# Performance work log

Hardware: AMD Instinct MI355X
Metric: run time of the kernel (lower is better)

Reference implementation:

```python
import jax, jax.numpy as jnp
import numpy as np

N_SITES = 64
N_HALF = N_SITES // 2
D_BOND = 128
N_OUTPUT = 10
DIM = 2
BATCH = 128


def _initializer(key, n_sites, d_phys, d_bond):
    # identity cores + small noise, matching the numpy initializer
    w = jnp.broadcast_to(jnp.eye(d_bond, dtype=jnp.float32),
                         (d_phys, n_sites, d_bond, d_bond))
    return w + 0.01 * jax.random.normal(key, w.shape, dtype=jnp.float32)


def setup_inputs() -> dict:
    key = jax.random.key(0)
    k_in, k_l, k_r, k_m = jax.random.split(key, 4)
    inputs = jax.random.normal(k_in, (BATCH, N_SITES, DIM), dtype=jnp.float32)
    left = _initializer(k_l, N_HALF, DIM, D_BOND)            # [dim, n_half, D, D]
    right = _initializer(k_r, N_HALF, DIM, D_BOND)           # [dim, n_half, D, D]
    middle = _initializer(k_m, 1, N_OUTPUT, D_BOND)[:, 0]    # [n_output, D, D]
    return {"inputs": inputs, "left": left, "right": right, "middle": middle}


def _reduction(t):
    # t: [size, B, D, D] -> [B, D, D] via balanced binary-tree matmul chain
    size = t.shape[0]
    while size > 1:
        half = size // 2
        nice = 2 * half
        leftover = t[nice:]
        t = jnp.matmul(t[0:nice:2], t[1:nice:2])  # [half, B, D, D]
        if leftover.shape[0]:
            t = jnp.concatenate([t, leftover], axis=0)
        size = half + (size % 2)
    return t[0]


def reference(inputs, left, right, middle):
    n_half = left.shape[1]
    # contract physical legs: [dim, l, D, D] x [B, l, dim] -> [l, B, D, D]
    l = jnp.einsum('slij,bls->lbij', left, inputs[:, :n_half])
    r = jnp.einsum('slij,bls->lbij', right, inputs[:, n_half:])
    l = _reduction(l)  # [B, D, D]
    r = _reduction(r)  # [B, D, D]
    # close the ring through the output core
    return jnp.einsum('bij,cjk,bki->bc', l, middle, r)  # [B, n_output]
```

## Files before the change

### kernel.cpp

```cpp
#include <hip/hip_runtime.h>


typedef __attribute__((ext_vector_type(8))) short short8v;
typedef __attribute__((ext_vector_type(16))) float f32x16;

__device__ __forceinline__ unsigned cvt_pk_bf16(float lo, float hi) {
  unsigned r;
  asm("v_cvt_pk_bf16_f32 %0, %1, %2" : "=v"(r) : "v"(lo), "v"(hi));
  return r;
}

#define GLOAD_LDS16(g, l)                                          \
  __builtin_amdgcn_global_load_lds(                                \
      (const __attribute__((address_space(1))) void*)(g),          \
      (__attribute__((address_space(3))) void*)(l), 16, 0, 0)

__global__ __launch_bounds__(256) void make_dt(const float* __restrict__ left,
                                               const float* __restrict__ right,
                                               ushort* __restrict__ Dt) {
  __shared__ float lw[64 * 132];
  const int tid = threadIdx.x;
  const int mat = blockIdx.x >> 1;
  const int rh  = blockIdx.x & 1;
  const float* W = (mat >= 64 ? right : left) + (size_t)(mat & 63) * 16384 +
                   (size_t)rh * 8192;

#pragma unroll
  for (int it = 0; it < 8; ++it) {
    int g = it * 256 + tid;
    float4 v = *(const float4*)(W + g * 4);
    *(float4*)&lw[(g >> 5) * 132 + (g & 31) * 4] = v;
  }
  __syncthreads();

#pragma unroll
  for (int ff = 0; ff < 4; ++ff) {
    int f = ff * 256 + tid;
    int l = f & 63, mt = (f >> 6) & 3, ksl = f >> 8;
    int m = 32 * mt + (l & 31);
    int kbl = 16 * ksl + 8 * (l >> 5);
    float v[8];
#pragma unroll
    for (int j = 0; j < 8; ++j)
      v[j] = lw[(kbl + j) * 132 + m] - ((64 * rh + kbl + j == m) ? 1.0f : 0.0f);
    uint4 o;
    o.x = cvt_pk_bf16(v[0], v[1]);
    o.y = cvt_pk_bf16(v[2], v[3]);
    o.z = cvt_pk_bf16(v[4], v[5]);
    o.w = cvt_pk_bf16(v[6], v[7]);
    *(uint4*)(Dt + (size_t)mat * 16384 +
              (size_t)(((4 * rh + ksl) * 4 + mt) * 64 + l) * 8) = o;
  }
}

__global__ __launch_bounds__(256, 1) void mps_chain_mfma(
    const float* __restrict__ inp, const float* __restrict__ left,
    const float* __restrict__ right, const ushort* __restrict__ Dt,
    float* __restrict__ res) {
  __shared__ ushort ldsD[2][32768];
  __shared__ float xs[64];

  const int tid  = threadIdx.x;
  const int half = blockIdx.x >> 7;
  const int b    = blockIdx.x & 127;
  const int lane = tid & 63;
  const int w    = tid >> 6;
  const int c    = lane & 31;
  const int hi   = lane >> 5;
  const int cg   = 32 * w + c;
  const int wofs = w * 512;

  if (tid < 64) xs[tid] = inp[b * 128 + half * 64 + tid];

  const ushort* DtH = Dt + (size_t)(half * 2) * 32 * 16384;

  __syncthreads();

#pragma unroll
  for (int p = 0; p < 2; ++p) {
    const ushort* gp = DtH + (size_t)(p * 32 + 1) * 16384;
#pragma unroll
    for (int i = 0; i < 8; ++i)
      GLOAD_LDS16(gp + i * 2048 + wofs + lane * 8,
                  &ldsD[0][p * 16384 + i * 2048 + wofs]);
  }

  f32x16 acc[4];

  {
    const float* Wg = half ? right : left;
    const float x0 = xs[0], x1 = xs[1];
#pragma unroll
    for (int t = 0; t < 4; ++t)
#pragma unroll
      for (int g = 0; g < 4; ++g) {
        const int row = 32 * t + 8 * g + 4 * hi;
        const float4 w0 = *(const float4*)(Wg + cg * 128 + row);
        const float4 w1 = *(const float4*)(Wg + 32 * 16384 + cg * 128 + row);
        acc[t][4 * g + 0] = x0 * w0.x + x1 * w1.x;
        acc[t][4 * g + 1] = x0 * w0.y + x1 * w1.y;
        acc[t][4 * g + 2] = x0 * w0.z + x1 * w1.z;
        acc[t][4 * g + 3] = x0 * w0.w + x1 * w1.w;
      }
  }

  __syncthreads();

  int cur = 0;
  for (int s = 1; s < 32; ++s) {
    const float x0 = xs[2 * s], x1 = xs[2 * s + 1];
    const float s01 = x0 + x1;

    if (s < 31) {
#pragma unroll
      for (int p = 0; p < 2; ++p) {
        const ushort* gp = DtH + (size_t)(p * 32 + s + 1) * 16384;
#pragma unroll
        for (int i = 0; i < 8; ++i)
          GLOAD_LDS16(gp + i * 2048 + wofs + lane * 8,
                      &ldsD[cur ^ 1][p * 16384 + i * 2048 + wofs]);
      }
    }

    f32x16 tn[4];
#pragma unroll
    for (int t = 0; t < 4; ++t)
#pragma unroll
      for (int r = 0; r < 16; ++r) tn[t][r] = s01 * acc[t][r];

#pragma unroll
    for (int ks = 0; ks < 8; ++ks) {
      const int t = ks >> 1, q = ks & 1;
#pragma unroll
      for (int r = 0; r < 4; ++r) {
        float a  = acc[t][q * 8 + r];
        float b2 = acc[t][q * 8 + 4 + r];
        asm volatile("v_permlane32_swap_b32 %0, %1" : "+v"(a), "+v"(b2));
        acc[t][q * 8 + r]     = a;
        acc[t][q * 8 + 4 + r] = b2;
      }
      uint4 p0, p1;
      {
        const float* v = (const float*)&acc[t] + q * 8;
        p0.x = cvt_pk_bf16(x0 * v[0], x0 * v[1]);
        p0.y = cvt_pk_bf16(x0 * v[2], x0 * v[3]);
        p0.z = cvt_pk_bf16(x0 * v[4], x0 * v[5]);
        p0.w = cvt_pk_bf16(x0 * v[6], x0 * v[7]);
        p1.x = cvt_pk_bf16(x1 * v[0], x1 * v[1]);
        p1.y = cvt_pk_bf16(x1 * v[2], x1 * v[3]);
        p1.z = cvt_pk_bf16(x1 * v[4], x1 * v[5]);
        p1.w = cvt_pk_bf16(x1 * v[6], x1 * v[7]);
      }
      const short8v y0 = __builtin_bit_cast(short8v, p0);
      const short8v y1 = __builtin_bit_cast(short8v, p1);
#pragma unroll
      for (int mt = 0; mt < 4; ++mt) {
        short8v d0 = *(const short8v*)&ldsD[cur][(ks * 4 + mt) * 512 + lane * 8];
        short8v d1 = *(const short8v*)&ldsD[cur][16384 + (ks * 4 + mt) * 512 + lane * 8];
        tn[mt] = __builtin_amdgcn_mfma_f32_32x32x16_bf16(d0, y0, tn[mt], 0, 0, 0);
        tn[mt] = __builtin_amdgcn_mfma_f32_32x32x16_bf16(d1, y1, tn[mt], 0, 0, 0);
      }
    }

#pragma unroll
    for (int t = 0; t < 4; ++t) acc[t] = tn[t];
    __syncthreads();
    cur ^= 1;
  }

  float* O = res + (size_t)(half * 128 + b) * 16384;
#pragma unroll
  for (int t = 0; t < 4; ++t)
#pragma unroll
    for (int g = 0; g < 4; ++g) {
      const int row = 32 * t + 8 * g + 4 * hi;
      float4 o = {acc[t][4 * g + 0], acc[t][4 * g + 1], acc[t][4 * g + 2],
                  acc[t][4 * g + 3]};
      *(float4*)(O + cg * 128 + row) = o;
    }
}

#define TS 132

__global__ __launch_bounds__(256) void mps_final(const float* __restrict__ res,
                                                 const float* __restrict__ middle,
                                                 float* __restrict__ out) {
  __shared__ float lA[128 * TS];
  __shared__ float lB[128 * TS];
  __shared__ float red[4][10];

  const int tid = threadIdx.x;
  const int b   = blockIdx.x;
  const float* Rg = res + (size_t)(128 + b) * 16384;
  const float* Lg = res + (size_t)b * 16384;

#pragma unroll
  for (int it = 0; it < 16; ++it) {
    int g = it * 256 + tid;
    int row = g >> 5, col = (g & 31) * 4;
    *(float4*)&lA[row * TS + col] = *(const float4*)(Rg + g * 4);
    *(float4*)&lB[row * TS + col] = *(const float4*)(Lg + g * 4);
  }
  __syncthreads();

  const int ty = tid >> 4, tx = tid & 15;
  const int k0 = ty * 8, j0 = tx * 8;

  float ct[8][8];
#pragma unroll
  for (int i = 0; i < 8; ++i)
#pragma unroll
    for (int j = 0; j < 8; ++j) ct[i][j] = 0.f;

  for (int k = 0; k < 128; k += 4) {
    float4 a[8];
#pragma unroll
    for (int i = 0; i < 8; ++i)
      a[i] = *(const float4*)&lA[(k0 + i) * TS + k];
    float4 b0[4], b1[4];
#pragma unroll
    for (int kk = 0; kk < 4; ++kk) {
      b0[kk] = *(const float4*)&lB[(k + kk) * TS + j0];
      b1[kk] = *(const float4*)&lB[(k + kk) * TS + j0 + 4];
    }
#pragma unroll
    for (int i = 0; i < 8; ++i) {
      const float av[4] = {a[i].x, a[i].y, a[i].z, a[i].w};
#pragma unroll
      for (int kk = 0; kk < 4; ++kk) {
        const float aa = av[kk];
        ct[i][0] = fmaf(aa, b0[kk].x, ct[i][0]);
        ct[i][1] = fmaf(aa, b0[kk].y, ct[i][1]);
        ct[i][2] = fmaf(aa, b0[kk].z, ct[i][2]);
        ct[i][3] = fmaf(aa, b0[kk].w, ct[i][3]);
        ct[i][4] = fmaf(aa, b1[kk].x, ct[i][4]);
        ct[i][5] = fmaf(aa, b1[kk].y, ct[i][5]);
        ct[i][6] = fmaf(aa, b1[kk].z, ct[i][6]);
        ct[i][7] = fmaf(aa, b1[kk].w, ct[i][7]);
      }
    }
  }
#pragma unroll
  for (int cc = 0; cc < 10; ++cc) {
    const float* m = middle + cc * 16384;
    float accv = 0.f;
#pragma unroll
    for (int jj = 0; jj < 8; ++jj) {
      const float* mr = m + (j0 + jj) * 128 + k0;
      float4 m0 = *(const float4*)(mr);
      float4 m1 = *(const float4*)(mr + 4);
      accv += m0.x * ct[0][jj] + m0.y * ct[1][jj] + m0.z * ct[2][jj] + m0.w * ct[3][jj];
      accv += m1.x * ct[4][jj] + m1.y * ct[5][jj] + m1.z * ct[6][jj] + m1.w * ct[7][jj];
    }
    float v = accv;
#pragma unroll
    for (int off = 32; off > 0; off >>= 1) v += __shfl_down(v, off);
    if ((tid & 63) == 0) red[tid >> 6][cc] = v;
  }
  __syncthreads();
  if (tid < 10)
    out[b * 10 + tid] = red[0][tid] + red[1][tid] + red[2][tid] + red[3][tid];
}

extern "C" void kernel_launch(void* const* d_in, const int* in_sizes, int n_in,
                              void* d_out, int out_size, void* d_ws, size_t ws_size,
                              hipStream_t stream) {
  const float* inputs = (const float*)d_in[0];
  const float* left   = (const float*)d_in[1];
  const float* right  = (const float*)d_in[2];
  const float* middle = (const float*)d_in[3];
  float* out = (float*)d_out;

  float*  res = (float*)d_ws;
  ushort* Dt  = (ushort*)((char*)d_ws + (size_t)16 * 1024 * 1024);

  make_dt<<<256, 256, 0, stream>>>(left, right, Dt);
  make_dt<<<256, 256, 0, stream>>>(left, right, Dt);
  mps_chain_mfma<<<256, 256, 0, stream>>>(inputs, left, right, Dt, res);
  mps_final<<<128, 256, 0, stream>>>(res, middle, out);
}
```

Before: 181.4 us.

## Split chain K-dimension across 8 waves with LDS partial-sum exchange

The chain kernel now runs 512 threads per block, with two wave groups each computing half the K-dimension of every step's matmul. Partial products are swapped through an LDS exchange buffer and summed, with two barriers per step. The double-buffered D tiles become a single buffer that is refilled after the first barrier, so loads overlap less with compute. The duplicate make_dt launch is also removed.

```diff
diff --git a/kernel.cpp b/kernel.cpp
--- a/kernel.cpp
+++ b/kernel.cpp
@@ -53,11 +53,23 @@
   }
 }
 
-__global__ __launch_bounds__(256, 1) void mps_chain_mfma(
+__device__ __forceinline__ void stage_D(const ushort* __restrict__ DtH, int s,
+                                        ushort* ldsD, int tid, int w) {
+#pragma unroll
+  for (int i = 0; i < 8; ++i) {
+    const int p = i >> 2;
+    const ushort* g =
+        DtH + (size_t)(p * 32 + s) * 16384 + (i & 3) * 4096 + tid * 8;
+    GLOAD_LDS16(g, ldsD + i * 4096 + w * 512);
+  }
+}
+
+__global__ __launch_bounds__(512, 1) void mps_chain_mfma(
     const float* __restrict__ inp, const float* __restrict__ left,
     const float* __restrict__ right, const ushort* __restrict__ Dt,
     float* __restrict__ res) {
-  __shared__ ushort ldsD[2][32768];
+  __shared__ __align__(16) ushort ldsD[32768];
+  __shared__ __align__(16) float exch[16384];
   __shared__ float xs[64];
 
   const int tid  = threadIdx.x;
@@ -65,83 +77,75 @@
   const int b    = blockIdx.x & 127;
   const int lane = tid & 63;
   const int w    = tid >> 6;
-  const int c    = lane & 31;
+  const int ct   = w & 3;
+  const int rh   = w >> 2;
   const int hi   = lane >> 5;
-  const int cg   = 32 * w + c;
-  const int wofs = w * 512;
+  const int cg   = 32 * ct + (lane & 31);
 
   if (tid < 64) xs[tid] = inp[b * 128 + half * 64 + tid];
 
   const ushort* DtH = Dt + (size_t)(half * 2) * 32 * 16384;
 
+  stage_D(DtH, 1, ldsD, tid, w);
+
   __syncthreads();
 
-#pragma unroll
-  for (int p = 0; p < 2; ++p) {
-    const ushort* gp = DtH + (size_t)(p * 32 + 1) * 16384;
-#pragma unroll
-    for (int i = 0; i < 8; ++i)
-      GLOAD_LDS16(gp + i * 2048 + wofs + lane * 8,
-                  &ldsD[0][p * 16384 + i * 2048 + wofs]);
-  }
-
-  f32x16 acc[4];
-
+  f32x16 accL[2];
   {
     const float* Wg = half ? right : left;
     const float x0 = xs[0], x1 = xs[1];
 #pragma unroll
-    for (int t = 0; t < 4; ++t)
+    for (int tl = 0; tl < 2; ++tl)
 #pragma unroll
       for (int g = 0; g < 4; ++g) {
-        const int row = 32 * t + 8 * g + 4 * hi;
+        const int row = 64 * rh + 32 * tl + 8 * g + 4 * hi;
         const float4 w0 = *(const float4*)(Wg + cg * 128 + row);
         const float4 w1 = *(const float4*)(Wg + 32 * 16384 + cg * 128 + row);
-        acc[t][4 * g + 0] = x0 * w0.x + x1 * w1.x;
-        acc[t][4 * g + 1] = x0 * w0.y + x1 * w1.y;
-        acc[t][4 * g + 2] = x0 * w0.z + x1 * w1.z;
-        acc[t][4 * g + 3] = x0 * w0.w + x1 * w1.w;
-      }
-  }
-
-  __syncthreads();
-
-  int cur = 0;
+        accL[tl][4 * g + 0] = x0 * w0.x + x1 * w1.x;
+        accL[tl][4 * g + 1] = x0 * w0.y + x1 * w1.y;
+        accL[tl][4 * g + 2] = x0 * w0.z + x1 * w1.z;
+        accL[tl][4 * g + 3] = x0 * w0.w + x1 * w1.w;
+      }
+  }
+
+#pragma unroll 1
   for (int s = 1; s < 32; ++s) {
     const float x0 = xs[2 * s], x1 = xs[2 * s + 1];
     const float s01 = x0 + x1;
 
-    if (s < 31) {
-#pragma unroll
-      for (int p = 0; p < 2; ++p) {
-        const ushort* gp = DtH + (size_t)(p * 32 + s + 1) * 16384;
-#pragma unroll
-        for (int i = 0; i < 8; ++i)
-          GLOAD_LDS16(gp + i * 2048 + wofs + lane * 8,
-                      &ldsD[cur ^ 1][p * 16384 + i * 2048 + wofs]);
-      }
-    }
-
-    f32x16 tn[4];
-#pragma unroll
-    for (int t = 0; t < 4; ++t)
-#pragma unroll
-      for (int r = 0; r < 16; ++r) tn[t][r] = s01 * acc[t][r];
-
-#pragma unroll
-    for (int ks = 0; ks < 8; ++ks) {
-      const int t = ks >> 1, q = ks & 1;
+    f32x16 pp[4];
+    if (rh == 0) {
+#pragma unroll
+      for (int r = 0; r < 16; ++r) {
+        pp[0][r] = s01 * accL[0][r];
+        pp[1][r] = s01 * accL[1][r];
+        pp[2][r] = 0.f;
+        pp[3][r] = 0.f;
+      }
+    } else {
+#pragma unroll
+      for (int r = 0; r < 16; ++r) {
+        pp[0][r] = 0.f;
+        pp[1][r] = 0.f;
+        pp[2][r] = s01 * accL[0][r];
+        pp[3][r] = s01 * accL[1][r];
+      }
+    }
+
+#pragma unroll
+    for (int ksl = 0; ksl < 4; ++ksl) {
+      const int tl = ksl >> 1, q = ksl & 1;
 #pragma unroll
       for (int r = 0; r < 4; ++r) {
-        float a  = acc[t][q * 8 + r];
-        float b2 = acc[t][q * 8 + 4 + r];
+        float a  = accL[tl][q * 8 + r];
+        float b2 = accL[tl][q * 8 + 4 + r];
         asm volatile("v_permlane32_swap_b32 %0, %1" : "+v"(a), "+v"(b2));
-        acc[t][q * 8 + r]     = a;
-        acc[t][q * 8 + 4 + r] = b2;
+        accL[tl][q * 8 + r]     = a;
+        accL[tl][q * 8 + 4 + r] = b2;
       }
       uint4 p0, p1;
       {
-        const float* v = (const float*)&acc[t] + q * 8;
+        const float* v = (const float*)&accL[tl] + q * 8;
         p0.x = cvt_pk_bf16(x0 * v[0], x0 * v[1]);
         p0.y = cvt_pk_bf16(x0 * v[2], x0 * v[3]);
         p0.z = cvt_pk_bf16(x0 * v[4], x0 * v[5]);
@@ -153,29 +157,79 @@
       }
       const short8v y0 = __builtin_bit_cast(short8v, p0);
       const short8v y1 = __builtin_bit_cast(short8v, p1);
+      const int ks = 4 * rh + ksl;
 #pragma unroll
       for (int mt = 0; mt < 4; ++mt) {
-        short8v d0 = *(const short8v*)&ldsD[cur][(ks * 4 + mt) * 512 + lane * 8];
-        short8v d1 = *(const short8v*)&ldsD[cur][16384 + (ks * 4 + mt) * 512 + lane * 8];
-        tn[mt] = __builtin_amdgcn_mfma_f32_32x32x16_bf16(d0, y0, tn[mt], 0, 0, 0);
-        tn[mt] = __builtin_amdgcn_mfma_f32_32x32x16_bf16(d1, y1, tn[mt], 0, 0, 0);
-      }
-    }
-
-#pragma unroll
-    for (int t = 0; t < 4; ++t) acc[t] = tn[t];
+        short8v d0 = *(const short8v*)&ldsD[(ks * 4 + mt) * 512 + lane * 8];
+        short8v d1 = *(const short8v*)&ldsD[16384 + (ks * 4 + mt) * 512 + lane * 8];
+        pp[mt] = __builtin_amdgcn_mfma_f32_32x32x16_bf16(d0, y0, pp[mt], 0, 0, 0);
+        pp[mt] = __builtin_amdgcn_mfma_f32_32x32x16_bf16(d1, y1, pp[mt], 0, 0, 0);
+      }
+    }
+
+    {
+      float* wb = exch + w * 2048 + lane * 4;
+      if (rh == 0) {
+#pragma unroll
+        for (int tl2 = 0; tl2 < 2; ++tl2)
+#pragma unroll
+          for (int g = 0; g < 4; ++g) {
+            float4 val = {pp[2 + tl2][4 * g + 0], pp[2 + tl2][4 * g + 1],
+                          pp[2 + tl2][4 * g + 2], pp[2 + tl2][4 * g + 3]};
+            *(float4*)(wb + (tl2 * 4 + g) * 256) = val;
+          }
+      } else {
+#pragma unroll
+        for (int tl2 = 0; tl2 < 2; ++tl2)
+#pragma unroll
+          for (int g = 0; g < 4; ++g) {
+            float4 val = {pp[tl2][4 * g + 0], pp[tl2][4 * g + 1],
+                          pp[tl2][4 * g + 2], pp[tl2][4 * g + 3]};
+            *(float4*)(wb + (tl2 * 4 + g) * 256) = val;
+          }
+      }
+    }
     __syncthreads();
-    cur ^= 1;
+
+    if (s < 31) stage_D(DtH, s + 1, ldsD, tid, w);
+
+    {
+      const float* rb = exch + (w ^ 4) * 2048 + lane * 4;
+      if (rh == 0) {
+#pragma unroll
+        for (int tl2 = 0; tl2 < 2; ++tl2)
+#pragma unroll
+          for (int g = 0; g < 4; ++g) {
+            float4 e = *(const float4*)(rb + (tl2 * 4 + g) * 256);
+            accL[tl2][4 * g + 0] = pp[tl2][4 * g + 0] + e.x;
+            accL[tl2][4 * g + 1] = pp[tl2][4 * g + 1] + e.y;
+            accL[tl2][4 * g + 2] = pp[tl2][4 * g + 2] + e.z;
+            accL[tl2][4 * g + 3] = pp[tl2][4 * g + 3] + e.w;
+          }
+      } else {
+#pragma unroll
+        for (int tl2 = 0; tl2 < 2; ++tl2)
+#pragma unroll
+          for (int g = 0; g < 4; ++g) {
+            float4 e = *(const float4*)(rb + (tl2 * 4 + g) * 256);
+            accL[tl2][4 * g + 0] = pp[2 + tl2][4 * g + 0] + e.x;
+            accL[tl2][4 * g + 1] = pp[2 + tl2][4 * g + 1] + e.y;
+            accL[tl2][4 * g + 2] = pp[2 + tl2][4 * g + 2] + e.z;
+            accL[tl2][4 * g + 3] = pp[2 + tl2][4 * g + 3] + e.w;
+          }
+      }
+    }
+    __syncthreads();
   }
 
   float* O = res + (size_t)(half * 128 + b) * 16384;
 #pragma unroll
-  for (int t = 0; t < 4; ++t)
+  for (int tl = 0; tl < 2; ++tl)
 #pragma unroll
     for (int g = 0; g < 4; ++g) {
-      const int row = 32 * t + 8 * g + 4 * hi;
-      float4 o = {acc[t][4 * g + 0], acc[t][4 * g + 1], acc[t][4 * g + 2],
-                  acc[t][4 * g + 3]};
+      const int row = 64 * rh + 32 * tl + 8 * g + 4 * hi;
+      float4 o = {accL[tl][4 * g + 0], accL[tl][4 * g + 1],
+                  accL[tl][4 * g + 2], accL[tl][4 * g + 3]};
       *(float4*)(O + cg * 128 + row) = o;
     }
 }
@@ -275,7 +329,6 @@
   ushort* Dt  = (ushort*)((char*)d_ws + (size_t)16 * 1024 * 1024);
 
   make_dt<<<256, 256, 0, stream>>>(left, right, Dt);
-  make_dt<<<256, 256, 0, stream>>>(left, right, Dt);
-  mps_chain_mfma<<<256, 256, 0, stream>>>(inputs, left, right, Dt, res);
+  mps_chain_mfma<<<256, 512, 0, stream>>>(inputs, left, right, Dt, res);
   mps_final<<<128, 256, 0, stream>>>(res, middle, out);
 }
```

After: 189.2 us. 4.3% more time.

## Pre-combine per-site deviation matrices so each step issues one MFMA per tile

Applied to the files above, without the earlier changes.

Each block now forms the input-weighted site matrix x0*D0 + x1*D1 in bf16 while loading it through registers, then writes that single combined matrix to LDS. The chain step then does one MFMA per tile instead of two and packs only one B operand. This halves MFMA work and LDS footprint. In exchange, the direct global-to-LDS loads become register loads plus VALU unpack and combine work. Rounding the combined matrix to bf16 adds a small precision change. The duplicated make_dt launch is also removed.

```diff
diff --git a/kernel.cpp b/kernel.cpp
--- a/kernel.cpp
+++ b/kernel.cpp
@@ -10,10 +10,23 @@
   return r;
 }
 
-#define GLOAD_LDS16(g, l)                                          \
-  __builtin_amdgcn_global_load_lds(                                \
-      (const __attribute__((address_space(1))) void*)(g),          \
-      (__attribute__((address_space(3))) void*)(l), 16, 0, 0)
+__device__ __forceinline__ unsigned combine_u(unsigned a, unsigned b, float x0,
+                                              float x1) {
+  float al = __builtin_bit_cast(float, a << 16);
+  float ah = __builtin_bit_cast(float, a & 0xffff0000u);
+  float bl = __builtin_bit_cast(float, b << 16);
+  float bh = __builtin_bit_cast(float, b & 0xffff0000u);
+  return cvt_pk_bf16(fmaf(x0, al, x1 * bl), fmaf(x0, ah, x1 * bh));
+}
+
+__device__ __forceinline__ uint4 combine4(uint4 a, uint4 b, float x0, float x1) {
+  uint4 o;
+  o.x = combine_u(a.x, b.x, x0, x1);
+  o.y = combine_u(a.y, b.y, x0, x1);
+  o.z = combine_u(a.z, b.z, x0, x1);
+  o.w = combine_u(a.w, b.w, x0, x1);
+  return o;
+}
 
 __global__ __launch_bounds__(256) void make_dt(const float* __restrict__ left,
                                                const float* __restrict__ right,
@@ -57,7 +70,7 @@
     const float* __restrict__ inp, const float* __restrict__ left,
     const float* __restrict__ right, const ushort* __restrict__ Dt,
     float* __restrict__ res) {
-  __shared__ ushort ldsD[2][32768];
+  __shared__ __align__(16) ushort ldsE[2][16384];
   __shared__ float xs[64];
 
   const int tid  = threadIdx.x;
@@ -65,25 +78,15 @@
   const int b    = blockIdx.x & 127;
   const int lane = tid & 63;
   const int w    = tid >> 6;
-  const int c    = lane & 31;
   const int hi   = lane >> 5;
-  const int cg   = 32 * w + c;
-  const int wofs = w * 512;
+  const int cg   = 32 * w + (lane & 31);
 
   if (tid < 64) xs[tid] = inp[b * 128 + half * 64 + tid];
 
-  const ushort* DtH = Dt + (size_t)(half * 2) * 32 * 16384;
-
-  __syncthreads();
-
-#pragma unroll
-  for (int p = 0; p < 2; ++p) {
-    const ushort* gp = DtH + (size_t)(p * 32 + 1) * 16384;
-#pragma unroll
-    for (int i = 0; i < 8; ++i)
-      GLOAD_LDS16(gp + i * 2048 + wofs + lane * 8,
-                  &ldsD[0][p * 16384 + i * 2048 + wofs]);
-  }
+  const ushort* D0 = Dt + (size_t)(half * 2) * 32 * 16384;
+  const ushort* D1 = D0 + (size_t)32 * 16384;
+
+  __syncthreads();
 
   f32x16 acc[4];
 
@@ -104,21 +107,36 @@
       }
   }
 
+  {
+    const float x0 = xs[2], x1 = xs[3];
+    const ushort* g0 = D0 + 16384;
+    const ushort* g1 = D1 + 16384;
+#pragma unroll
+    for (int i = 0; i < 8; ++i) {
+      const int slot = i * 256 + tid;
+      uint4 a = *(const uint4*)(g0 + slot * 8);
+      uint4 bb = *(const uint4*)(g1 + slot * 8);
+      *(uint4*)&ldsE[0][slot * 8] = combine4(a, bb, x0, x1);
+    }
+  }
   __syncthreads();
 
   int cur = 0;
+#pragma unroll 1
   for (int s = 1; s < 32; ++s) {
     const float x0 = xs[2 * s], x1 = xs[2 * s + 1];
     const float s01 = x0 + x1;
-
+    const ushort* bufC = ldsE[cur];
+
+    uint4 ga[8], gb[8];
     if (s < 31) {
-#pragma unroll
-      for (int p = 0; p < 2; ++p) {
-        const ushort* gp = DtH + (size_t)(p * 32 + s + 1) * 16384;
-#pragma unroll
-        for (int i = 0; i < 8; ++i)
-          GLOAD_LDS16(gp + i * 2048 + wofs + lane * 8,
-                      &ldsD[cur ^ 1][p * 16384 + i * 2048 + wofs]);
+      const ushort* g0 = D0 + (size_t)(s + 1) * 16384;
+      const ushort* g1 = D1 + (size_t)(s + 1) * 16384;
+#pragma unroll
+      for (int i = 0; i < 8; ++i) {
+        const int slot = i * 256 + tid;
+        ga[i] = *(const uint4*)(g0 + slot * 8);
+        gb[i] = *(const uint4*)(g1 + slot * 8);
       }
     }
 
@@ -139,26 +157,29 @@
         acc[t][q * 8 + r]     = a;
         acc[t][q * 8 + 4 + r] = b2;
       }
-      uint4 p0, p1;
+      uint4 py;
       {
         const float* v = (const float*)&acc[t] + q * 8;
-        p0.x = cvt_pk_bf16(x0 * v[0], x0 * v[1]);
-        p0.y = cvt_pk_bf16(x0 * v[2], x0 * v[3]);
-        p0.z = cvt_pk_bf16(x0 * v[4], x0 * v[5]);
-        p0.w = cvt_pk_bf16(x0 * v[6], x0 * v[7]);
-        p1.x = cvt_pk_bf16(x1 * v[0], x1 * v[1]);
-        p1.y = cvt_pk_bf16(x1 * v[2], x1 * v[3]);
-        p1.z = cvt_pk_bf16(x1 * v[4], x1 * v[5]);
-        p1.w = cvt_pk_bf16(x1 * v[6], x1 * v[7]);
-      }
-      const short8v y0 = __builtin_bit_cast(short8v, p0);
-      const short8v y1 = __builtin_bit_cast(short8v, p1);
+        py.x = cvt_pk_bf16(v[0], v[1]);
+        py.y = cvt_pk_bf16(v[2], v[3]);
+        py.z = cvt_pk_bf16(v[4], v[5]);
+        py.w = cvt_pk_bf16(v[6], v[7]);
+      }
+      const short8v y = __builtin_bit_cast(short8v, py);
 #pragma unroll
       for (int mt = 0; mt < 4; ++mt) {
-        short8v d0 = *(const short8v*)&ldsD[cur][(ks * 4 + mt) * 512 + lane * 8];
-        short8v d1 = *(const short8v*)&ldsD[cur][16384 + (ks * 4 + mt) * 512 + lane * 8];
-        tn[mt] = __builtin_amdgcn_mfma_f32_32x32x16_bf16(d0, y0, tn[mt], 0, 0, 0);
-        tn[mt] = __builtin_amdgcn_mfma_f32_32x32x16_bf16(d1, y1, tn[mt], 0, 0, 0);
+        short8v e = *(const short8v*)&bufC[(ks * 4 + mt) * 512 + lane * 8];
+        tn[mt] = __builtin_amdgcn_mfma_f32_32x32x16_bf16(e, y, tn[mt], 0, 0, 0);
+      }
+    }
+
+    if (s < 31) {
+      const float xn0 = xs[2 * s + 2], xn1 = xs[2 * s + 3];
+      ushort* bufN = ldsE[cur ^ 1];
+#pragma unroll
+      for (int i = 0; i < 8; ++i) {
+        const int slot = i * 256 + tid;
+        *(uint4*)&bufN[slot * 8] = combine4(ga[i], gb[i], xn0, xn1);
       }
     }
 
@@ -275,7 +296,6 @@
   ushort* Dt  = (ushort*)((char*)d_ws + (size_t)16 * 1024 * 1024);
 
   make_dt<<<256, 256, 0, stream>>>(left, right, Dt);
-  make_dt<<<256, 256, 0, stream>>>(left, right, Dt);
   mps_chain_mfma<<<256, 256, 0, stream>>>(inputs, left, right, Dt, res);
   mps_final<<<128, 256, 0, stream>>>(res, middle, out);
 }
```

Measured after the change: 183.7 us. Within noise of the previous version (+1.3%).
